# Performance work log

Measured on AMD Instinct MI355X. Metric: run time of the kernel, lower is better.

The kernel has to match this reference:

```python
import jax, jax.numpy as jnp
import numpy as np

N_NODES = 100000


def gcn_conv(x, edge_index, W, b):
    """PyG GCNConv: add self-loops, symmetric deg^{-1/2} normalization,
    linear transform, scatter-add aggregation, then bias."""
    n = x.shape[0]
    loops = jnp.arange(n, dtype=edge_index.dtype)
    src = jnp.concatenate([edge_index[0], loops])  # [E+N]
    dst = jnp.concatenate([edge_index[1], loops])  # [E+N]
    # degree (with self-loops) of each target node
    deg = jax.ops.segment_sum(jnp.ones_like(dst, dtype=x.dtype), dst, num_segments=n)
    dinv = jnp.where(deg > 0, jax.lax.rsqrt(deg), 0.0)
    norm = dinv[src] * dinv[dst]  # [E+N]
    h = x @ W  # [N, out_dim] -- transform before aggregation
    msg = h[src] * norm[:, None]  # gather + normalize
    out = jax.ops.segment_sum(msg, dst, num_segments=n)  # scatter-add
    return out + b


def setup_inputs() -> dict:
    key = jax.random.key(0)
    ks = jax.random.split(key, 8)
    n, e, d_in, d_h = N_NODES, 1600000, 32, 64
    x = jax.random.normal(ks[0], (n, d_in), dtype=jnp.float32)
    edge_index = jax.random.randint(ks[1], (2, e), 0, n, dtype=jnp.int64)
    # Glorot-style init for GCN weights, uniform for linear layer
    W1 = jax.random.normal(ks[2], (d_in, d_h), dtype=jnp.float32) / np.sqrt(d_in)
    b1 = jnp.zeros((d_h,), dtype=jnp.float32)
    W2 = jax.random.normal(ks[3], (d_h, d_h), dtype=jnp.float32) / np.sqrt(d_h)
    b2 = jnp.zeros((d_h,), dtype=jnp.float32)
    Wo = jax.random.normal(ks[4], (d_h, 1), dtype=jnp.float32) / np.sqrt(d_h)
    bo = jnp.zeros((1,), dtype=jnp.float32)
    return {"x": x, "edge_index": edge_index, "W1": W1, "b1": b1,
            "W2": W2, "b2": b2, "Wo": Wo, "bo": bo}


def reference(x, edge_index, W1, b1, W2, b2, Wo, bo):
    h = jax.nn.relu(gcn_conv(x, edge_index, W1, b1))
    h = jax.nn.relu(gcn_conv(h, edge_index, W2, b2))
    logits = h @ Wo + bo  # [N, 1]
    return jax.nn.sigmoid(logits).squeeze(-1)  # [N]
```

## Files before the change

kernel.cpp:

```cpp
#include <hip/hip_runtime.h>

#define DH 64
#define DIN 32
#define BSH 8
#define BNODES 256
#define MAXB 1024
#define CAPSH 13
#define CAP (1 << CAPSH)

typedef unsigned short u16;
typedef unsigned int u32;

__device__ __forceinline__ float bf2f(u16 u) {
    union { u32 i; float f; } x; x.i = ((u32)u) << 16; return x.f;
}
__device__ __forceinline__ u16 f2bf(float f) {
    union { float f; u32 i; } x; x.f = f;
    u32 r = x.i + 0x7fff + ((x.i >> 16) & 1);
    return (u16)(r >> 16);
}

__global__ void __launch_bounds__(256) binA_k(
        const int* __restrict__ ei, int* __restrict__ gcnt,
        u32* __restrict__ pairs, int E, int n, int nbuck) {
    __shared__ int lhist[MAXB];
    __shared__ int lbase[MAXB];
    __shared__ int smode;
    int t = threadIdx.x;
    if (t < 64) {
        int v = (2 * t + 1 < 2 * E) ? ei[2 * t + 1] : 0;
        unsigned long long b = __ballot(v != 0);
        if (t == 0) smode = (b != 0ULL) ? 1 : 0;
    }
    for (int b = t; b < nbuck; b += 256) lhist[b] = 0;
    __syncthreads();
    int m = smode;
    unsigned un = (unsigned)n;
    int q0 = blockIdx.x * 256 + t;
    int qs = gridDim.x * 256;

    if (m && !(E & 3)) {
        const int4* d4 = (const int4*)(ei + E);
        for (int q = q0; q < (E >> 2); q += qs) {
            int4 d = d4[q];
            if ((unsigned)d.x < un) atomicAdd(&lhist[d.x >> BSH], 1);
            if ((unsigned)d.y < un) atomicAdd(&lhist[d.y >> BSH], 1);
            if ((unsigned)d.z < un) atomicAdd(&lhist[d.z >> BSH], 1);
            if ((unsigned)d.w < un) atomicAdd(&lhist[d.w >> BSH], 1);
        }
    } else if (!m && !(E & 1)) {
        const int4* d4 = (const int4*)(ei + 2 * E);
        for (int q = q0; q < (E >> 1); q += qs) {
            int4 d = d4[q];
            if ((unsigned)d.x < un) atomicAdd(&lhist[d.x >> BSH], 1);
            if ((unsigned)d.z < un) atomicAdd(&lhist[d.z >> BSH], 1);
        }
    } else {
        const int* dstp = m ? (ei + E) : (ei + 2 * E);
        int stride = m ? 1 : 2;
        for (int e = q0; e < E; e += qs) {
            int d = dstp[(size_t)e * stride];
            if ((unsigned)d < un) atomicAdd(&lhist[d >> BSH], 1);
        }
    }
    __syncthreads();
    for (int b = t; b < nbuck; b += 256) {
        int c = lhist[b];
        lbase[b] = c ? ((b << CAPSH) + atomicAdd(&gcnt[b], c)) : 0;
        lhist[b] = 0;
    }
    __syncthreads();
    #define EMIT(S, D)                                                     \
        if ((unsigned)(D) < un) {                                          \
            int sv = ((unsigned)(S) < un) ? (S) : 0;                       \
            int bb = (D) >> BSH;                                           \
            int off = atomicAdd(&lhist[bb], 1);                            \
            int pos = lbase[bb] + off;                                     \
            if (pos < ((bb + 1) << CAPSH))                                 \
                pairs[pos] = ((u32)sv << BSH) | (u32)((D) & (BNODES - 1)); \
        }
    if (m && !(E & 3)) {
        const int4* s4 = (const int4*)ei;
        const int4* d4 = (const int4*)(ei + E);
        for (int q = q0; q < (E >> 2); q += qs) {
            int4 s = s4[q]; int4 d = d4[q];
            EMIT(s.x, d.x) EMIT(s.y, d.y) EMIT(s.z, d.z) EMIT(s.w, d.w)
        }
    } else if (!m && !(E & 1)) {
        const int4* s4 = (const int4*)ei;
        const int4* d4 = (const int4*)(ei + 2 * E);
        for (int q = q0; q < (E >> 1); q += qs) {
            int4 s = s4[q]; int4 d = d4[q];
            EMIT(s.x, d.x) EMIT(s.z, d.z)
        }
    } else {
        const int* srcp = ei;
        const int* dstp = m ? (ei + E) : (ei + 2 * E);
        int stride = m ? 1 : 2;
        for (int e = q0; e < E; e += qs) {
            int d = dstp[(size_t)e * stride];
            int s = srcp[(size_t)e * stride];
            EMIT(s, d)
        }
    }
    #undef EMIT
}

__global__ void __launch_bounds__(512) csr_bucket_k(
        const u32* __restrict__ pairs, const int* __restrict__ gcnt,
        int* __restrict__ rstart, int* __restrict__ rend,
        int* __restrict__ col, float* __restrict__ dinv, int N) {
    __shared__ int cnt[BNODES];
    __shared__ int s[BNODES];
    int b = blockIdx.x, t = threadIdx.x;
    int base = b << CAPSH;
    int ec = gcnt[b]; if (ec > CAP) ec = CAP;
    int end = base + ec;
    if (t < BNODES) cnt[t] = 0;
    __syncthreads();
    for (int i = base + t; i < end; i += 512)
        atomicAdd(&cnt[pairs[i] & (BNODES - 1)], 1);
    __syncthreads();
    int v = (t < BNODES) ? cnt[t] : 0;
    if (t < BNODES) s[t] = v;
    __syncthreads();
    for (int off = 1; off < BNODES; off <<= 1) {
        int x = (t >= off && t < BNODES) ? s[t - off] : 0;
        __syncthreads();
        if (t < BNODES) s[t] += x;
        __syncthreads();
    }
    if (t < BNODES) {
        int excl = s[t] - v;
        int a = base + excl;
        int node = (b << BSH) + t;
        if (node < N) {
            rstart[node] = a;
            rend[node]   = a + v;
            dinv[node]   = rsqrtf((float)v + 1.0f);
        }
        cnt[t] = a;
    }
    __syncthreads();
    for (int i = base + t; i < end; i += 512) {
        u32 p = pairs[i];
        int pos = atomicAdd(&cnt[p & (BNODES - 1)], 1);
        col[pos] = (int)(p >> BSH);
    }
}

__global__ void __launch_bounds__(256) gemm1_k(
        const float* __restrict__ x, const float* __restrict__ W1,
        const float* __restrict__ dinv, u16* __restrict__ hp, int n) {
    __shared__ float Wl[DIN * DH];
    __shared__ float xl[16][DIN + 4];
    int tid = threadIdx.x;
    {
        const float4* Wv = (const float4*)W1;
        float4* Wd = (float4*)Wl;
        Wd[tid] = Wv[tid];
        Wd[tid + 256] = Wv[tid + 256];
    }
    int lane = tid & 63, w = tid >> 6;
    int g = lane >> 4, c = lane & 15;
    for (int sub = 0; sub < 4; sub++) {
        int tb = blockIdx.x * 64 + sub * 16;
        __syncthreads();
        if (tid < 128) {
            int idx = tid * 4;
            int row = idx / DIN, ck = idx % DIN;
            float4 v = {0.f, 0.f, 0.f, 0.f};
            if (tb + row < n)
                v = *(const float4*)&x[(size_t)(tb + row) * DIN + ck];
            *(float4*)&xl[row][ck] = v;
        }
        __syncthreads();
        int node = tb + w * 4 + g;
        const float* xr = xl[w * 4 + g];
        float4 acc = {0.f, 0.f, 0.f, 0.f};
        #pragma unroll
        for (int k = 0; k < DIN; k++) {
            float xv = xr[k];
            float4 wv = *(const float4*)&Wl[k * DH + c * 4];
            acc.x += xv * wv.x; acc.y += xv * wv.y; acc.z += xv * wv.z; acc.w += xv * wv.w;
        }
        if (node < n) {
            float di = dinv[node];
            ushort4 o;
            o.x = f2bf(acc.x * di); o.y = f2bf(acc.y * di);
            o.z = f2bf(acc.z * di); o.w = f2bf(acc.w * di);
            *(ushort4*)&hp[(size_t)node * DH + c * 4] = o;
        }
    }
}

__device__ __forceinline__ float4 edge_sum_grp(const u16* __restrict__ hp,
                                               const int* __restrict__ col,
                                               int start, int deg, int g, int c) {
    int dm = deg;
    dm = max(dm, __shfl_xor(dm, 16, 64));
    dm = max(dm, __shfl_xor(dm, 32, 64));
    float4 acc = {0.f, 0.f, 0.f, 0.f};
    if (dm <= 0) return acc;
    int gl = g << 4;
    int cb = (c < deg) ? col[start + c] : 0;
    for (int base = 0; base < dm; base += 16) {
        int nb = base + 16;
        int cbn = 0;
        if (nb < dm) cbn = (nb + c < deg) ? col[start + nb + c] : 0;
        int rm = dm - base; if (rm > 16) rm = 16;
        for (int j = 0; j < rm; j += 4) {
            int s0 = __shfl(cb, gl | j, 64);
            int s1 = __shfl(cb, gl | (j + 1), 64);
            int s2 = __shfl(cb, gl | (j + 2), 64);
            int s3 = __shfl(cb, gl | (j + 3), 64);
            bool a0 = base + j     < deg;
            bool a1 = base + j + 1 < deg;
            bool a2 = base + j + 2 < deg;
            bool a3 = base + j + 3 < deg;
            ushort4 v0, v1, v2, v3;
            if (a0) v0 = *(const ushort4*)&hp[(size_t)s0 * DH + c * 4];
            if (a1) v1 = *(const ushort4*)&hp[(size_t)s1 * DH + c * 4];
            if (a2) v2 = *(const ushort4*)&hp[(size_t)s2 * DH + c * 4];
            if (a3) v3 = *(const ushort4*)&hp[(size_t)s3 * DH + c * 4];
            if (a0) { acc.x += bf2f(v0.x); acc.y += bf2f(v0.y); acc.z += bf2f(v0.z); acc.w += bf2f(v0.w); }
            if (a1) { acc.x += bf2f(v1.x); acc.y += bf2f(v1.y); acc.z += bf2f(v1.z); acc.w += bf2f(v1.w); }
            if (a2) { acc.x += bf2f(v2.x); acc.y += bf2f(v2.y); acc.z += bf2f(v2.z); acc.w += bf2f(v2.w); }
            if (a3) { acc.x += bf2f(v3.x); acc.y += bf2f(v3.y); acc.z += bf2f(v3.z); acc.w += bf2f(v3.w); }
        }
        cb = cbn;
    }
    return acc;
}

__global__ void __launch_bounds__(256) agg_gemm_k(
        const u16* __restrict__ hp, const int* __restrict__ rstart,
        const int* __restrict__ rend, const int* __restrict__ col,
        const float* __restrict__ dinv, const float* __restrict__ b1,
        const float* __restrict__ W2, u16* __restrict__ hp2, int N) {
    __shared__ float Wl[DH * DH];
    __shared__ float xs[4][4][DH + 4];
    int tid = threadIdx.x;
    {
        const float4* Wv = (const float4*)W2;
        float4* Wd = (float4*)Wl;
        #pragma unroll
        for (int r = 0; r < 4; r++) Wd[tid + 256 * r] = Wv[tid + 256 * r];
    }
    __syncthreads();
    int lane = tid & 63, w = tid >> 6;
    int g = lane >> 4, c = lane & 15;
    int node = blockIdx.x * 16 + w * 4 + g;
    int start = 0, deg = 0;
    if (node < N) { start = rstart[node]; deg = rend[node] - start; }
    float4 acc = edge_sum_grp(hp, col, start, deg, g, c);
    float di = (node < N) ? dinv[node] : 0.f;
    float4 o = {0.f, 0.f, 0.f, 0.f};
    if (node < N) {
        ushort4 sv = *(const ushort4*)&hp[(size_t)node * DH + c * 4];
        float4 b = *(const float4*)&b1[c * 4];
        o.x = fmaxf((acc.x + bf2f(sv.x)) * di + b.x, 0.f);
        o.y = fmaxf((acc.y + bf2f(sv.y)) * di + b.y, 0.f);
        o.z = fmaxf((acc.z + bf2f(sv.z)) * di + b.z, 0.f);
        o.w = fmaxf((acc.w + bf2f(sv.w)) * di + b.w, 0.f);
    }
    *(float4*)&xs[w][g][c * 4] = o;
    const float* xr = xs[w][g];
    float4 a2 = {0.f, 0.f, 0.f, 0.f};
    #pragma unroll
    for (int k = 0; k < DH; k++) {
        float xv = xr[k];
        float4 wv = *(const float4*)&Wl[k * DH + c * 4];
        a2.x += xv * wv.x; a2.y += xv * wv.y; a2.z += xv * wv.z; a2.w += xv * wv.w;
    }
    if (node < N) {
        ushort4 po;
        po.x = f2bf(a2.x * di); po.y = f2bf(a2.y * di);
        po.z = f2bf(a2.z * di); po.w = f2bf(a2.w * di);
        *(ushort4*)&hp2[(size_t)node * DH + c * 4] = po;
    }
}

__global__ void __launch_bounds__(256) agg_head_k(
        const u16* __restrict__ hp, const int* __restrict__ rstart,
        const int* __restrict__ rend, const int* __restrict__ col,
        const float* __restrict__ dinv, const float* __restrict__ bias,
        const float* __restrict__ Wo, const float* __restrict__ bo,
        float* __restrict__ y, int N) {
    int lane = threadIdx.x & 63;
    int g = lane >> 4, c = lane & 15;
    int node = blockIdx.x * 16 + (threadIdx.x >> 6) * 4 + g;
    int start = 0, deg = 0;
    if (node < N) { start = rstart[node]; deg = rend[node] - start; }
    float4 acc = edge_sum_grp(hp, col, start, deg, g, c);
    float t = 0.f;
    if (node < N) {
        ushort4 sv = *(const ushort4*)&hp[(size_t)node * DH + c * 4];
        float4 b = *(const float4*)&bias[c * 4];
        float4 wo = *(const float4*)&Wo[c * 4];
        float di = dinv[node];
        t = fmaxf((acc.x + bf2f(sv.x)) * di + b.x, 0.f) * wo.x
          + fmaxf((acc.y + bf2f(sv.y)) * di + b.y, 0.f) * wo.y
          + fmaxf((acc.z + bf2f(sv.z)) * di + b.z, 0.f) * wo.z
          + fmaxf((acc.w + bf2f(sv.w)) * di + b.w, 0.f) * wo.w;
    }
    #pragma unroll
    for (int m = 1; m < 16; m <<= 1) t += __shfl_xor(t, m, 64);
    if (c == 0 && node < N) {
        float z = t + bo[0];
        y[node] = 1.f / (1.f + __expf(-z));
    }
}

extern "C" void kernel_launch(void* const* d_in, const int* in_sizes, int n_in,
                              void* d_out, int out_size, void* d_ws, size_t ws_size,
                              hipStream_t stream) {
    const float* x  = (const float*)d_in[0];
    const int*   ei = (const int*)d_in[1];
    const float* W1 = (const float*)d_in[2];
    const float* b1 = (const float*)d_in[3];
    const float* W2 = (const float*)d_in[4];
    const float* b2 = (const float*)d_in[5];
    const float* Wo = (const float*)d_in[6];
    const float* bo = (const float*)d_in[7];
    float* y = (float*)d_out;

    int N = in_sizes[0] / DIN;
    int E = in_sizes[1] / 2;
    int nbuck = ((N - 1) >> BSH) + 1;

    char* ws = (char*)d_ws;
    size_t off = 0;
    auto alloc = [&](size_t bytes) { char* p = ws + off; off += (bytes + 255) & ~(size_t)255; return p; };
    int*   gcnt   = (int*)alloc(MAXB * 4);
    int*   rstart = (int*)alloc((size_t)N * 4);
    int*   rend   = (int*)alloc((size_t)N * 4);
    float* dinv   = (float*)alloc((size_t)N * 4);
    int*   col    = (int*)alloc(((size_t)nbuck << CAPSH) * 4);
    size_t pair_b = ((size_t)nbuck << CAPSH) * 4;
    size_t hp_b   = (size_t)N * DH * 2;
    char*  bufA   = (char*)alloc(pair_b > hp_b ? pair_b : hp_b);
    u16*   bufB   = (u16*)alloc(hp_b);
    u16*   hp    = (u16*)bufA;
    u32*   pairs = (u32*)bufA;

    int gN16 = (N + 15) / 16;
    int gN64 = (N + 63) / 64;

    hipMemsetAsync(gcnt, 0, (size_t)nbuck * 4, stream);
    binA_k<<<768, 256, 0, stream>>>(ei, gcnt, pairs, E, N, nbuck);
    csr_bucket_k<<<nbuck, 512, 0, stream>>>(pairs, gcnt, rstart, rend, col, dinv, N);

    gemm1_k<<<gN64, 256, 0, stream>>>(x, W1, dinv, hp, N);
    agg_gemm_k<<<gN16, 256, 0, stream>>>(hp, rstart, rend, col, dinv, b1, W2, bufB, N);
    agg_head_k<<<gN16, 256, 0, stream>>>(bufB, rstart, rend, col, dinv, b2, Wo, bo, y, N);
}
```

Baseline: 207.6 us.

## Fuse CSR bucketing with first GEMM and unroll edge gather by eight

The first-layer transform x@W1 now runs inside the CSR bucket kernel. Each block computes h for its 256 nodes using the dinv values it keeps in shared memory, and writes the bf16 result over its own, already consumed, slice of the pairs buffer. This removes one kernel launch and the global reload of dinv, at the cost of heavier blocks and fewer blocks for the GEMM work. The neighbour-gather loop also issues 8 row loads per step instead of 4, to keep more memory requests in flight.

```diff
diff --git a/kernel.cpp b/kernel.cpp
--- a/kernel.cpp
+++ b/kernel.cpp
@@ -106,16 +106,21 @@
     #undef EMIT
 }
 
-__global__ void __launch_bounds__(512) csr_bucket_k(
-        const u32* __restrict__ pairs, const int* __restrict__ gcnt,
+__global__ void __launch_bounds__(512) csr_gemm_k(
+        u32* __restrict__ pairs, const int* __restrict__ gcnt,
         int* __restrict__ rstart, int* __restrict__ rend,
-        int* __restrict__ col, float* __restrict__ dinv, int N) {
+        int* __restrict__ col, float* __restrict__ dinv,
+        const float* __restrict__ x, const float* __restrict__ W1, int N) {
     __shared__ int cnt[BNODES];
     __shared__ int s[BNODES];
+    __shared__ float dl[BNODES];
+    __shared__ float Wl[DIN * DH];
+    __shared__ float xl[32][DIN + 4];
     int b = blockIdx.x, t = threadIdx.x;
     int base = b << CAPSH;
     int ec = gcnt[b]; if (ec > CAP) ec = CAP;
     int end = base + ec;
+    ((float4*)Wl)[t] = ((const float4*)W1)[t];
     if (t < BNODES) cnt[t] = 0;
     __syncthreads();
     for (int i = base + t; i < end; i += 512)
@@ -125,19 +130,21 @@
     if (t < BNODES) s[t] = v;
     __syncthreads();
     for (int off = 1; off < BNODES; off <<= 1) {
-        int x = (t >= off && t < BNODES) ? s[t - off] : 0;
+        int xsc = (t >= off && t < BNODES) ? s[t - off] : 0;
         __syncthreads();
-        if (t < BNODES) s[t] += x;
+        if (t < BNODES) s[t] += xsc;
         __syncthreads();
     }
     if (t < BNODES) {
         int excl = s[t] - v;
         int a = base + excl;
         int node = (b << BSH) + t;
+        float di = rsqrtf((float)v + 1.0f);
+        dl[t] = di;
         if (node < N) {
             rstart[node] = a;
             rend[node]   = a + v;
-            dinv[node]   = rsqrtf((float)v + 1.0f);
+            dinv[node]   = di;
         }
         cnt[t] = a;
     }
@@ -147,36 +154,26 @@
         int pos = atomicAdd(&cnt[p & (BNODES - 1)], 1);
         col[pos] = (int)(p >> BSH);
     }
-}
-
-__global__ void __launch_bounds__(256) gemm1_k(
-        const float* __restrict__ x, const float* __restrict__ W1,
-        const float* __restrict__ dinv, u16* __restrict__ hp, int n) {
-    __shared__ float Wl[DIN * DH];
-    __shared__ float xl[16][DIN + 4];
-    int tid = threadIdx.x;
-    {
-        const float4* Wv = (const float4*)W1;
-        float4* Wd = (float4*)Wl;
-        Wd[tid] = Wv[tid];
-        Wd[tid + 256] = Wv[tid + 256];
-    }
-    int lane = tid & 63, w = tid >> 6;
+    __syncthreads();
+    u16* hp = (u16*)pairs;
+    int lane = t & 63, w = t >> 6;
     int g = lane >> 4, c = lane & 15;
-    for (int sub = 0; sub < 4; sub++) {
-        int tb = blockIdx.x * 64 + sub * 16;
+    for (int it = 0; it < 8; it++) {
+        int nl0 = it * 32;
         __syncthreads();
-        if (tid < 128) {
-            int idx = tid * 4;
+        if (t < 256) {
+            int idx = t * 4;
             int row = idx / DIN, ck = idx % DIN;
-            float4 v = {0.f, 0.f, 0.f, 0.f};
-            if (tb + row < n)
-                v = *(const float4*)&x[(size_t)(tb + row) * DIN + ck];
-            *(float4*)&xl[row][ck] = v;
+            int node = (b << BSH) + nl0 + row;
+            float4 vx = {0.f, 0.f, 0.f, 0.f};
+            if (node < N)
+                vx = *(const float4*)&x[(size_t)node * DIN + ck];
+            *(float4*)&xl[row][ck] = vx;
         }
         __syncthreads();
-        int node = tb + w * 4 + g;
-        const float* xr = xl[w * 4 + g];
+        int nl = nl0 + w * 4 + g;
+        int node = (b << BSH) + nl;
+        const float* xr = xl[nl - nl0];
         float4 acc = {0.f, 0.f, 0.f, 0.f};
         #pragma unroll
         for (int k = 0; k < DIN; k++) {
@@ -184,8 +181,8 @@
             float4 wv = *(const float4*)&Wl[k * DH + c * 4];
             acc.x += xv * wv.x; acc.y += xv * wv.y; acc.z += xv * wv.z; acc.w += xv * wv.w;
         }
-        if (node < n) {
-            float di = dinv[node];
+        if (node < N) {
+            float di = dl[nl];
             ushort4 o;
             o.x = f2bf(acc.x * di); o.y = f2bf(acc.y * di);
             o.z = f2bf(acc.z * di); o.w = f2bf(acc.w * di);
@@ -209,24 +206,40 @@
         int cbn = 0;
         if (nb < dm) cbn = (nb + c < deg) ? col[start + nb + c] : 0;
         int rm = dm - base; if (rm > 16) rm = 16;
-        for (int j = 0; j < rm; j += 4) {
+        for (int j = 0; j < rm; j += 8) {
             int s0 = __shfl(cb, gl | j, 64);
             int s1 = __shfl(cb, gl | (j + 1), 64);
             int s2 = __shfl(cb, gl | (j + 2), 64);
             int s3 = __shfl(cb, gl | (j + 3), 64);
+            int s4 = __shfl(cb, gl | (j + 4), 64);
+            int s5 = __shfl(cb, gl | (j + 5), 64);
+            int s6 = __shfl(cb, gl | (j + 6), 64);
+            int s7 = __shfl(cb, gl | (j + 7), 64);
             bool a0 = base + j     < deg;
             bool a1 = base + j + 1 < deg;
             bool a2 = base + j + 2 < deg;
             bool a3 = base + j + 3 < deg;
-            ushort4 v0, v1, v2, v3;
+            bool a4 = base + j + 4 < deg;
+            bool a5 = base + j + 5 < deg;
+            bool a6 = base + j + 6 < deg;
+            bool a7 = base + j + 7 < deg;
+            ushort4 v0, v1, v2, v3, v4, v5, v6, v7;
             if (a0) v0 = *(const ushort4*)&hp[(size_t)s0 * DH + c * 4];
             if (a1) v1 = *(const ushort4*)&hp[(size_t)s1 * DH + c * 4];
             if (a2) v2 = *(const ushort4*)&hp[(size_t)s2 * DH + c * 4];
             if (a3) v3 = *(const ushort4*)&hp[(size_t)s3 * DH + c * 4];
+            if (a4) v4 = *(const ushort4*)&hp[(size_t)s4 * DH + c * 4];
+            if (a5) v5 = *(const ushort4*)&hp[(size_t)s5 * DH + c * 4];
+            if (a6) v6 = *(const ushort4*)&hp[(size_t)s6 * DH + c * 4];
+            if (a7) v7 = *(const ushort4*)&hp[(size_t)s7 * DH + c * 4];
             if (a0) { acc.x += bf2f(v0.x); acc.y += bf2f(v0.y); acc.z += bf2f(v0.z); acc.w += bf2f(v0.w); }
             if (a1) { acc.x += bf2f(v1.x); acc.y += bf2f(v1.y); acc.z += bf2f(v1.z); acc.w += bf2f(v1.w); }
             if (a2) { acc.x += bf2f(v2.x); acc.y += bf2f(v2.y); acc.z += bf2f(v2.z); acc.w += bf2f(v2.w); }
             if (a3) { acc.x += bf2f(v3.x); acc.y += bf2f(v3.y); acc.z += bf2f(v3.z); acc.w += bf2f(v3.w); }
+            if (a4) { acc.x += bf2f(v4.x); acc.y += bf2f(v4.y); acc.z += bf2f(v4.z); acc.w += bf2f(v4.w); }
+            if (a5) { acc.x += bf2f(v5.x); acc.y += bf2f(v5.y); acc.z += bf2f(v5.z); acc.w += bf2f(v5.w); }
+            if (a6) { acc.x += bf2f(v6.x); acc.y += bf2f(v6.y); acc.z += bf2f(v6.z); acc.w += bf2f(v6.w); }
+            if (a7) { acc.x += bf2f(v7.x); acc.y += bf2f(v7.y); acc.z += bf2f(v7.z); acc.w += bf2f(v7.w); }
         }
         cb = cbn;
     }
@@ -345,13 +358,10 @@
     u32*   pairs = (u32*)bufA;
 
     int gN16 = (N + 15) / 16;
-    int gN64 = (N + 63) / 64;
 
     hipMemsetAsync(gcnt, 0, (size_t)nbuck * 4, stream);
     binA_k<<<768, 256, 0, stream>>>(ei, gcnt, pairs, E, N, nbuck);
-    csr_bucket_k<<<nbuck, 512, 0, stream>>>(pairs, gcnt, rstart, rend, col, dinv, N);
-
-    gemm1_k<<<gN64, 256, 0, stream>>>(x, W1, dinv, hp, N);
+    csr_gemm_k<<<nbuck, 512, 0, stream>>>(pairs, gcnt, rstart, rend, col, dinv, x, W1, N);
     agg_gemm_k<<<gN16, 256, 0, stream>>>(hp, rstart, rend, col, dinv, b1, W2, bufB, N);
     agg_head_k<<<gN16, 256, 0, stream>>>(bufB, rstart, rend, col, dinv, b2, Wo, bo, y, N);
 }
```

After: 200.1 us (median of 2 runs). 1.04x faster.
